# Kernel tuning notes

Measured on AMD Instinct MI355X. Metric: run time of the kernel, lower is better.

Reference implementation:

```python
import jax, jax.numpy as jnp
import numpy as np

B, T, D = 4, 2048, 1024
DEPTH = 4
LEAF_DIM = 256
NUM_LEAVES = 2 ** DEPTH          # 16
NUM_NODES = NUM_LEAVES - 1       # 15


def _uniform(key, shape, scale):
    s = 1.0 / np.sqrt(scale)
    return jax.random.uniform(key, shape, minval=-s, maxval=s, dtype=jnp.float32)


def setup_inputs() -> dict:
    key = jax.random.key(0)
    ks = jax.random.split(key, 8)
    x = jax.random.normal(ks[0], (B, T, D), dtype=jnp.float32)
    # gate params: Dense(1) per internal node, level-order layout
    node_w = _uniform(ks[1], (NUM_NODES, D), D)
    node_b = _uniform(ks[2], (NUM_NODES,), D)
    # leaf MLP params: D -> LEAF_DIM -> D, stacked over leaves
    w1 = _uniform(ks[3], (NUM_LEAVES, D, LEAF_DIM), D)
    b1 = _uniform(ks[4], (NUM_LEAVES, LEAF_DIM), D)
    w2 = _uniform(ks[5], (NUM_LEAVES, LEAF_DIM, D), LEAF_DIM)
    b2 = _uniform(ks[6], (NUM_LEAVES, D), LEAF_DIM)
    return {"x": x, "node_w": node_w, "node_b": node_b,
            "w1": w1, "b1": b1, "w2": w2, "b2": b2, "training": 0}


def _leaf_probs(x, node_w, node_b, depth):
    # gate activations for all internal nodes at once: [B,T,NUM_NODES]
    c = jax.nn.sigmoid(jnp.einsum('btd,nd->btn', x, node_w) + node_b)
    probs = jnp.ones(c.shape[:-1] + (1,), dtype=c.dtype)
    for m in range(depth):
        start = 2 ** m - 1
        cl = c[..., start:start + 2 ** m]          # gates at level m: [B,T,2^m]
        # left child gets c, right child gets (1-c); interleave preserves
        # the recursion's n -> (2n, 2n+1) indexing
        probs = jnp.stack([probs * cl, probs * (1.0 - cl)], axis=-1)
        probs = probs.reshape(probs.shape[:-2] + (-1,))
    return probs                                   # [B,T,NUM_LEAVES]


def reference(x, node_w, node_b, w1, b1, w2, b2, training):
    num_leaves = w1.shape[0]
    depth = int(np.log2(num_leaves))
    probs = _leaf_probs(x, node_w, node_b, depth)          # [B,T,L]
    # all leaf MLP hidden layers as one batched GEMM
    h = jax.nn.relu(jnp.einsum('btd,ldh->btlh', x, w1) + b1)
    # weight hidden by leaf probability, then contract l and h together so the
    # [B,T,L,D] per-leaf output is never materialized
    h = h * probs[..., None]
    out = jnp.einsum('btlh,lhd->btd', h, w2)
    out = out + jnp.einsum('btl,ld->btd', probs, b2)
    return out
```

## Files before the change

### kernel.cpp

```cpp
#include <hip/hip_runtime.h>
#include <stdint.h>

typedef unsigned short ushort_t;
typedef __bf16 bf16x8 __attribute__((ext_vector_type(8)));
typedef float f32x4 __attribute__((ext_vector_type(4)));

#define M_TOK 8192
#define K1 1024
#define N1 4096
#define K2 4160
#define N2 1024

__device__ __forceinline__ ushort_t f2bf(float f) {
  union { float f; unsigned u; } v; v.f = f;
  unsigned u = v.u;
  u += 0x7FFFu + ((u >> 16) & 1u);
  return (ushort_t)(u >> 16);
}

__device__ __forceinline__ void gload16(const void* g, void* l) {
  __builtin_amdgcn_global_load_lds((__attribute__((address_space(1))) void*)g,
                                   (__attribute__((address_space(3))) void*)l,
                                   16, 0, 0);
}

__global__ __launch_bounds__(256) void k_probs(
    const float* __restrict__ x, const float* __restrict__ node_w,
    const float* __restrict__ node_b, ushort_t* __restrict__ xb,
    float* __restrict__ probs, ushort_t* __restrict__ hp) {
  const int wid = threadIdx.x >> 6, lane = threadIdx.x & 63;
  const int t = blockIdx.x * 4 + wid;
  const float* xr = x + (size_t)t * K1;
  float xv[16];
#pragma unroll
  for (int j = 0; j < 4; ++j) {
    float4 v = *(const float4*)(xr + j * 256 + lane * 4);
    xv[4*j+0] = v.x; xv[4*j+1] = v.y; xv[4*j+2] = v.z; xv[4*j+3] = v.w;
  }
  ushort_t* xbr = xb + (size_t)t * K1;
#pragma unroll
  for (int j = 0; j < 4; ++j) {
    ushort4 o;
    o.x = f2bf(xv[4*j+0]); o.y = f2bf(xv[4*j+1]);
    o.z = f2bf(xv[4*j+2]); o.w = f2bf(xv[4*j+3]);
    *(ushort4*)(xbr + j * 256 + lane * 4) = o;
  }
  float c[15];
#pragma unroll
  for (int n = 0; n < 15; ++n) {
    float s = 0.f;
    const float* wr = node_w + n * K1;
#pragma unroll
    for (int j = 0; j < 4; ++j) {
      float4 w = *(const float4*)(wr + j * 256 + lane * 4);
      s += xv[4*j+0]*w.x + xv[4*j+1]*w.y + xv[4*j+2]*w.z + xv[4*j+3]*w.w;
    }
#pragma unroll
    for (int off = 32; off > 0; off >>= 1) s += __shfl_xor(s, off);
    float z = s + node_b[n];
    c[n] = 1.f / (1.f + __expf(-z));
  }
  if (lane < 16) {
    float p = 1.f;
#pragma unroll
    for (int m = 0; m < 4; ++m) {
      int jm = lane >> (4 - m);
      int node = (1 << m) - 1 + jm;
      int bit = (lane >> (3 - m)) & 1;
      p *= bit ? (1.f - c[node]) : c[node];
    }
    probs[t * 16 + lane] = p;
    hp[(size_t)t * K2 + 4096 + lane] = f2bf(p);
  }
  if (lane < 48) hp[(size_t)t * K2 + 4112 + lane] = 0;
}

__global__ __launch_bounds__(256) void k_w1t(const float* __restrict__ w1,
                                             ushort_t* __restrict__ w1t) {
  __shared__ ushort_t tile[64][68];
  const int b = blockIdx.x;
  const int l = b >> 6, rem = b & 63;
  const int kt = rem >> 2, ht = rem & 3;
  const float* in = w1 + (size_t)l * K1 * 256;
  const int tr = threadIdx.x >> 4;
  const int tc = (threadIdx.x & 15) * 4;
#pragma unroll
  for (int rr = 0; rr < 4; ++rr) {
    int r = tr + rr * 16;
    float4 v = *(const float4*)(in + (size_t)(kt * 64 + r) * 256 + ht * 64 + tc);
    tile[r][tc+0] = f2bf(v.x); tile[r][tc+1] = f2bf(v.y);
    tile[r][tc+2] = f2bf(v.z); tile[r][tc+3] = f2bf(v.w);
  }
  __syncthreads();
#pragma unroll
  for (int rr = 0; rr < 4; ++rr) {
    int oh = tr + rr * 16;
    ushort4 o;
    o.x = tile[tc+0][oh]; o.y = tile[tc+1][oh];
    o.z = tile[tc+2][oh]; o.w = tile[tc+3][oh];
    *(ushort4*)(w1t + (size_t)(l * 256 + ht * 64 + oh) * K1 + kt * 64 + tc) = o;
  }
}

__global__ __launch_bounds__(256) void k_w2t(const float* __restrict__ w2,
                                             ushort_t* __restrict__ w2t) {
  __shared__ ushort_t tile[64][68];
  const int b = blockIdx.x;
  const int l = b >> 6, rem = b & 63;
  const int ht = rem >> 4, dt = rem & 15;
  const float* in = w2 + (size_t)l * 256 * N2;
  const int tr = threadIdx.x >> 4;
  const int tc = (threadIdx.x & 15) * 4;
#pragma unroll
  for (int rr = 0; rr < 4; ++rr) {
    int r = tr + rr * 16;
    float4 v = *(const float4*)(in + (size_t)(ht * 64 + r) * N2 + dt * 64 + tc);
    tile[r][tc+0] = f2bf(v.x); tile[r][tc+1] = f2bf(v.y);
    tile[r][tc+2] = f2bf(v.z); tile[r][tc+3] = f2bf(v.w);
  }
  __syncthreads();
#pragma unroll
  for (int rr = 0; rr < 4; ++rr) {
    int od = tr + rr * 16;
    ushort4 o;
    o.x = tile[tc+0][od]; o.y = tile[tc+1][od];
    o.z = tile[tc+2][od]; o.w = tile[tc+3][od];
    *(ushort4*)(w2t + (size_t)(dt * 64 + od) * K2 + l * 256 + ht * 64 + tc) = o;
  }
}

__global__ __launch_bounds__(256) void k_b2pad(const float* __restrict__ b2,
                                               ushort_t* __restrict__ w2t) {
  int tid = blockIdx.x * 256 + threadIdx.x;
  int d = tid >> 6, cc = tid & 63;
  float v = (cc < 16) ? b2[cc * N2 + d] : 0.f;
  w2t[(size_t)d * K2 + 4096 + cc] = f2bf(v);
}

template <int NT, int LDA, int LDB, int BN, int MODE>
__global__ __launch_bounds__(512, 2) void k_gemm8(
    const ushort_t* __restrict__ A, const ushort_t* __restrict__ Bt,
    const float* __restrict__ probs, const float* __restrict__ b1,
    ushort_t* __restrict__ hp, float* __restrict__ out, int ntn) {
  constexpr int BHR = BN / 2;
  constexpr int WN = (BN == 256) ? 4 : 2;
  constexpr int WM = 8 / WN;
  constexpr int FH = 128 / (WM * 16);
  constexpr int PHN = (BN == 256) ? 4 : 2;
  constexpr int ABYTES = 128 * 128;
  constexpr int BBYTES = BHR * 128;

  extern __shared__ char lds[];
  const int tid = threadIdx.x;
  int bid = blockIdx.x;
  const int nwg = gridDim.x;
  bid = (bid & 7) * (nwg >> 3) + (bid >> 3);
  const int bm = bid / ntn, bn = bid % ntn;

  const int wid = tid >> 6, lane = tid & 63;
  const int widM = wid / WN, widN = wid % WN;
  const int wmBase = widM * (FH * 16);
  const int wn = widN * 64;
  const int lr = lane & 15, g = lane >> 4;

  const ushort_t* Ag = A + (size_t)bm * 256 * LDA;
  const ushort_t* Bg = Bt + (size_t)bn * BN * LDB;

  const int srow = tid >> 3;
  const int scol = ((tid & 7) << 4) ^ ((srow & 7) << 4);

  auto stageA = [&](int buf, int half, int kt) {
    const ushort_t* src = Ag + (size_t)(half * 128) * LDA + kt * 64;
    char* dst = lds + (buf * 2 + half) * ABYTES + tid * 16;
#pragma unroll
    for (int r = 0; r < 2; ++r)
      gload16((const char*)(src + (size_t)(srow + r * 64) * LDA) + scol,
              dst + r * 8192);
  };
  auto stageB = [&](int buf, int half, int kt) {
    const ushort_t* src = Bg + (size_t)(half * BHR) * LDB + kt * 64;
    char* dst = lds + 4 * ABYTES + (buf * 2 + half) * BBYTES + tid * 16;
#pragma unroll
    for (int r = 0; r < BHR / 64; ++r)
      gload16((const char*)(src + (size_t)(srow + r * 64) * LDB) + scol,
              dst + r * 8192);
  };
  auto rdA = [&](int buf, int half, int i, int kk) -> bf16x8 {
    int r = wmBase + i * 16 + lr;
    int off = r * 128 + (((kk * 4 + g) ^ (lr & 7)) << 4);
    return *(const bf16x8*)(lds + (buf * 2 + half) * ABYTES + off);
  };
  auto rdB = [&](int buf, int j, int kk) -> bf16x8 {
    int nr = wn + j * 16;
    int half = (nr >= BHR) ? 1 : 0;
    int r = (nr & (BHR - 1)) + lr;
    int off = r * 128 + (((kk * 4 + g) ^ (lr & 7)) << 4);
    return *(const bf16x8*)(lds + 4 * ABYTES + (buf * 2 + half) * BBYTES + off);
  };

  f32x4 acc[2 * FH][4];
#pragma unroll
  for (int i = 0; i < 2 * FH; ++i)
#pragma unroll
    for (int j = 0; j < 4; ++j) acc[i][j] = (f32x4){0.f, 0.f, 0.f, 0.f};

  stageA(0, 0, 0); stageA(0, 1, 0); stageB(0, 0, 0); stageB(0, 1, 0);
  stageA(1, 0, 1); stageB(1, 0, 1); stageB(1, 1, 1);
  if constexpr (BN == 256) asm volatile("s_waitcnt vmcnt(6)" ::: "memory");
  else                     asm volatile("s_waitcnt vmcnt(4)" ::: "memory");
  __builtin_amdgcn_sched_barrier(0);
  __builtin_amdgcn_s_barrier();

#pragma unroll 1
  for (int kt = 0; kt < NT; ++kt) {
    const int cur = kt & 1;
    bf16x8 bfr[2][4];
#pragma unroll
    for (int ph = 0; ph < PHN; ++ph) {
      constexpr int KKN = (PHN == 4) ? 1 : 2;
      const int q = (PHN == 4) ? (ph >> 1) : ph;
      bf16x8 af[FH][KKN];
#pragma unroll
      for (int kx = 0; kx < KKN; ++kx) {
        const int kk = (PHN == 4) ? (ph & 1) : kx;
#pragma unroll
        for (int i = 0; i < FH; ++i) af[i][kx] = rdA(cur, q, i, kk);
        if (q == 0) {
#pragma unroll
          for (int j = 0; j < 4; ++j) bfr[kk][j] = rdB(cur, j, kk);
        }
      }
      __builtin_amdgcn_sched_barrier(0x7);
      if constexpr (PHN == 4) {
        if (ph == 0 && kt + 1 < NT) stageA(cur ^ 1, 1, kt + 1);
        if (ph == 1 && kt + 2 < NT) stageA(cur, 0, kt + 2);
        if (ph == 2 && kt + 2 < NT) stageB(cur, 0, kt + 2);
        if (ph == 3 && kt + 2 < NT) stageB(cur, 1, kt + 2);
      } else {
        if (ph == 0 && kt + 1 < NT) stageA(cur ^ 1, 1, kt + 1);
        if (ph == 1 && kt + 2 < NT) {
          stageA(cur, 0, kt + 2);
          stageB(cur, 0, kt + 2); stageB(cur, 1, kt + 2);
        }
      }
      __builtin_amdgcn_s_barrier();
      __builtin_amdgcn_s_setprio(1);
#pragma unroll
      for (int kx = 0; kx < KKN; ++kx) {
        const int kk = (PHN == 4) ? (ph & 1) : kx;
#pragma unroll
        for (int i = 0; i < FH; ++i)
#pragma unroll
          for (int j = 0; j < 4; ++j)
            acc[q * FH + i][j] = __builtin_amdgcn_mfma_f32_16x16x32_bf16(
                af[i][kx], bfr[kk][j], acc[q * FH + i][j], 0, 0, 0);
      }
      __builtin_amdgcn_s_setprio(0);
      if (ph == PHN - 1) {
        if (kt + 2 < NT) {
          if constexpr (BN == 256) asm volatile("s_waitcnt vmcnt(6)" ::: "memory");
          else                     asm volatile("s_waitcnt vmcnt(4)" ::: "memory");
          __builtin_amdgcn_sched_barrier(0);
        } else if (kt + 1 < NT) {
          asm volatile("s_waitcnt vmcnt(0)" ::: "memory");
          __builtin_amdgcn_sched_barrier(0);
        }
      }
      __builtin_amdgcn_s_barrier();
    }
  }

  const int rowb = bm * 256 + wmBase + g * 4;
  const int colb = bn * BN + wn + lr;
  if (MODE == 0) {
    const int leaf = bn;
#pragma unroll
    for (int q = 0; q < 2; ++q)
#pragma unroll
      for (int i = 0; i < FH; ++i) {
        int rbase = rowb + q * 128 + i * 16;
        float pm[4];
#pragma unroll
        for (int rg = 0; rg < 4; ++rg)
          pm[rg] = probs[(size_t)(rbase + rg) * 16 + leaf];
#pragma unroll
        for (int j = 0; j < 4; ++j) {
          float bias = b1[colb + j * 16];
#pragma unroll
          for (int rg = 0; rg < 4; ++rg) {
            float v = acc[q * FH + i][j][rg] + bias;
            v = v > 0.f ? v : 0.f;
            v *= pm[rg];
            hp[(size_t)(rbase + rg) * K2 + colb + j * 16] = f2bf(v);
          }
        }
      }
  } else {
#pragma unroll
    for (int q = 0; q < 2; ++q)
#pragma unroll
      for (int i = 0; i < FH; ++i) {
        int rbase = rowb + q * 128 + i * 16;
#pragma unroll
        for (int j = 0; j < 4; ++j)
#pragma unroll
          for (int rg = 0; rg < 4; ++rg)
            out[(size_t)(rbase + rg) * N2 + colb + j * 16] = acc[q * FH + i][j][rg];
      }
  }
}

extern "C" void kernel_launch(void* const* d_in, const int* in_sizes, int n_in,
                              void* d_out, int out_size, void* d_ws, size_t ws_size,
                              hipStream_t stream) {
  const float* x      = (const float*)d_in[0];
  const float* node_w = (const float*)d_in[1];
  const float* node_b = (const float*)d_in[2];
  const float* w1     = (const float*)d_in[3];
  const float* b1     = (const float*)d_in[4];
  const float* w2     = (const float*)d_in[5];
  const float* b2     = (const float*)d_in[6];
  float* out = (float*)d_out;

  char* ws = (char*)d_ws;
  ushort_t* xb    = (ushort_t*)(ws);
  ushort_t* w1t   = (ushort_t*)(ws + 16777216);
  ushort_t* w2t   = (ushort_t*)(ws + 25165824);
  ushort_t* hp    = (ushort_t*)(ws + 33685504);
  float*    probs = (float*)   (ws + 101842944);

  k_probs<<<M_TOK / 4, 256, 0, stream>>>(x, node_w, node_b, xb, probs, hp);
  k_w1t<<<1024, 256, 0, stream>>>(w1, w1t);
  k_w2t<<<1024, 256, 0, stream>>>(w2, w2t);
  k_b2pad<<<256, 256, 0, stream>>>(b2, w2t);
  k_gemm8<16, K1, K1, 256, 0><<<512, 512, 131072, stream>>>(
      xb, w1t, probs, b1, hp, nullptr, N1 / 256);
  k_gemm8<65, K2, K2, 128, 1><<<256, 512, 98304, stream>>>(
      hp, w2t, nullptr, nullptr, nullptr, out, N2 / 128);
}
```

Measured before the change: 190.0 us.

## Restructure GEMM main loop into two half-tile phases with merged staging

Measured after the change: 184.2 us. 1.03x faster.

```diff
diff --git a/kernel.cpp b/kernel.cpp
--- a/kernel.cpp
+++ b/kernel.cpp
@@ -146,9 +146,9 @@
   constexpr int WN = (BN == 256) ? 4 : 2;
   constexpr int WM = 8 / WN;
   constexpr int FH = 128 / (WM * 16);
-  constexpr int PHN = (BN == 256) ? 4 : 2;
   constexpr int ABYTES = 128 * 128;
   constexpr int BBYTES = BHR * 128;
+  constexpr int KEEP = 2 + 2 * (BHR / 64);
 
   extern __shared__ char lds[];
   const int tid = threadIdx.x;
@@ -206,68 +206,77 @@
 
   stageA(0, 0, 0); stageA(0, 1, 0); stageB(0, 0, 0); stageB(0, 1, 0);
   stageA(1, 0, 1); stageB(1, 0, 1); stageB(1, 1, 1);
-  if constexpr (BN == 256) asm volatile("s_waitcnt vmcnt(6)" ::: "memory");
-  else                     asm volatile("s_waitcnt vmcnt(4)" ::: "memory");
+  {
+    constexpr int kp = KEEP;
+    if constexpr (kp == 6) asm volatile("s_waitcnt vmcnt(6)" ::: "memory");
+    else                   asm volatile("s_waitcnt vmcnt(4)" ::: "memory");
+  }
   __builtin_amdgcn_sched_barrier(0);
   __builtin_amdgcn_s_barrier();
+  __builtin_amdgcn_sched_barrier(0);
 
 #pragma unroll 1
   for (int kt = 0; kt < NT; ++kt) {
     const int cur = kt & 1;
     bf16x8 bfr[2][4];
-#pragma unroll
-    for (int ph = 0; ph < PHN; ++ph) {
-      constexpr int KKN = (PHN == 4) ? 1 : 2;
-      const int q = (PHN == 4) ? (ph >> 1) : ph;
-      bf16x8 af[FH][KKN];
-#pragma unroll
-      for (int kx = 0; kx < KKN; ++kx) {
-        const int kk = (PHN == 4) ? (ph & 1) : kx;
-#pragma unroll
-        for (int i = 0; i < FH; ++i) af[i][kx] = rdA(cur, q, i, kk);
-        if (q == 0) {
-#pragma unroll
-          for (int j = 0; j < 4; ++j) bfr[kk][j] = rdB(cur, j, kk);
-        }
+
+    {
+      bf16x8 a0[FH][2];
+#pragma unroll
+      for (int kk = 0; kk < 2; ++kk) {
+#pragma unroll
+        for (int i = 0; i < FH; ++i) a0[i][kk] = rdA(cur, 0, i, kk);
+#pragma unroll
+        for (int j = 0; j < 4; ++j) bfr[kk][j] = rdB(cur, j, kk);
       }
-      __builtin_amdgcn_sched_barrier(0x7);
-      if constexpr (PHN == 4) {
-        if (ph == 0 && kt + 1 < NT) stageA(cur ^ 1, 1, kt + 1);
-        if (ph == 1 && kt + 2 < NT) stageA(cur, 0, kt + 2);
-        if (ph == 2 && kt + 2 < NT) stageB(cur, 0, kt + 2);
-        if (ph == 3 && kt + 2 < NT) stageB(cur, 1, kt + 2);
-      } else {
-        if (ph == 0 && kt + 1 < NT) stageA(cur ^ 1, 1, kt + 1);
-        if (ph == 1 && kt + 2 < NT) {
-          stageA(cur, 0, kt + 2);
-          stageB(cur, 0, kt + 2); stageB(cur, 1, kt + 2);
-        }
+      if (kt + 1 < NT) stageA(cur ^ 1, 1, kt + 1);
+      __builtin_amdgcn_s_setprio(1);
+#pragma unroll
+      for (int kk = 0; kk < 2; ++kk)
+#pragma unroll
+        for (int i = 0; i < FH; ++i)
+#pragma unroll
+          for (int j = 0; j < 4; ++j)
+            acc[i][j] = __builtin_amdgcn_mfma_f32_16x16x32_bf16(
+                a0[i][kk], bfr[kk][j], acc[i][j], 0, 0, 0);
+      __builtin_amdgcn_s_setprio(0);
+    }
+    __builtin_amdgcn_s_barrier();
+    __builtin_amdgcn_sched_barrier(0);
+
+    {
+      bf16x8 a1[FH][2];
+#pragma unroll
+      for (int kk = 0; kk < 2; ++kk)
+#pragma unroll
+        for (int i = 0; i < FH; ++i) a1[i][kk] = rdA(cur, 1, i, kk);
+      if (kt + 2 < NT) {
+        stageA(cur, 0, kt + 2);
+        stageB(cur, 0, kt + 2);
+        stageB(cur, 1, kt + 2);
       }
-      __builtin_amdgcn_s_barrier();
       __builtin_amdgcn_s_setprio(1);
 #pragma unroll
-      for (int kx = 0; kx < KKN; ++kx) {
-        const int kk = (PHN == 4) ? (ph & 1) : kx;
+      for (int kk = 0; kk < 2; ++kk)
 #pragma unroll
         for (int i = 0; i < FH; ++i)
 #pragma unroll
           for (int j = 0; j < 4; ++j)
-            acc[q * FH + i][j] = __builtin_amdgcn_mfma_f32_16x16x32_bf16(
-                af[i][kx], bfr[kk][j], acc[q * FH + i][j], 0, 0, 0);
-      }
+            acc[FH + i][j] = __builtin_amdgcn_mfma_f32_16x16x32_bf16(
+                a1[i][kk], bfr[kk][j], acc[FH + i][j], 0, 0, 0);
       __builtin_amdgcn_s_setprio(0);
-      if (ph == PHN - 1) {
-        if (kt + 2 < NT) {
-          if constexpr (BN == 256) asm volatile("s_waitcnt vmcnt(6)" ::: "memory");
-          else                     asm volatile("s_waitcnt vmcnt(4)" ::: "memory");
-          __builtin_amdgcn_sched_barrier(0);
-        } else if (kt + 1 < NT) {
-          asm volatile("s_waitcnt vmcnt(0)" ::: "memory");
-          __builtin_amdgcn_sched_barrier(0);
-        }
-      }
-      __builtin_amdgcn_s_barrier();
-    }
+    }
+    if (kt + 2 < NT) {
+      constexpr int kp = KEEP;
+      if constexpr (kp == 6) asm volatile("s_waitcnt vmcnt(6)" ::: "memory");
+      else                   asm volatile("s_waitcnt vmcnt(4)" ::: "memory");
+      __builtin_amdgcn_sched_barrier(0);
+    } else if (kt + 1 < NT) {
+      asm volatile("s_waitcnt vmcnt(0)" ::: "memory");
+      __builtin_amdgcn_sched_barrier(0);
+    }
+    __builtin_amdgcn_s_barrier();
+    __builtin_amdgcn_sched_barrier(0);
   }
 
   const int rowb = bm * 256 + wmBase + g * 4;
```
